# Performance work log

Hardware: AMD Instinct MI355X
Metric: run time of the kernel (lower is better)

## Reference

```python
import jax, jax.numpy as jnp
import numpy as np

NUM_HEADS = 32
NUM_KV_HEADS = 8
HEAD_DIM = 128
SCALE = 1.0 / np.sqrt(128.0)
B = 8          # num sequences
LQ = 1024 // 8 # new (query) tokens per sequence
PAGE_SIZE = 16


def setup_inputs() -> dict:
    key = jax.random.key(0)
    ks = jax.random.split(key, 5)
    q = jax.random.normal(ks[0], (B * LQ, NUM_HEADS * HEAD_DIM), dtype=jnp.float32)
    k = jax.random.normal(ks[1], (B * LQ, NUM_KV_HEADS * HEAD_DIM), dtype=jnp.float32)
    v = jax.random.normal(ks[2], (B * LQ, NUM_KV_HEADS * HEAD_DIM), dtype=jnp.float32)
    k_cache = jax.random.normal(ks[3], (1024, PAGE_SIZE, NUM_KV_HEADS, HEAD_DIM), dtype=jnp.float32)
    v_cache = jax.random.normal(ks[4], (1024, PAGE_SIZE, NUM_KV_HEADS, HEAD_DIM), dtype=jnp.float32)
    page_tables = jnp.arange(8 * 128, dtype=jnp.int64).reshape(8, 128)  # distinct pages per seq
    return {"q": q, "k": k, "v": v, "k_cache": k_cache, "v_cache": v_cache,
            "page_tables": page_tables, "ctx_len": 2048, "block_size": 32}


def reference(q, k, v, k_cache, v_cache, page_tables, ctx_len, block_size):
    nh, nkvh, hd = NUM_HEADS, NUM_KV_HEADS, HEAD_DIM
    group = nh // nkvh
    # split flat token dim into [B, Lq]
    qs = q.reshape(B, LQ, nh, hd)
    k_new = k.reshape(B, LQ, nkvh, hd)
    v_new = v.reshape(B, LQ, nkvh, hd)
    # paged gather of cached context: [B, n_pages, P, nkvh, hd] -> [B, ctx_len, nkvh, hd]
    k_ctx = k_cache[page_tables].reshape(B, ctx_len, nkvh, hd)
    v_ctx = v_cache[page_tables].reshape(B, ctx_len, nkvh, hd)
    k_full = jnp.concatenate([k_ctx, k_new], axis=1)  # [B, ctx_len+Lq, nkvh, hd]
    v_full = jnp.concatenate([v_ctx, v_new], axis=1)
    # GQA: repeat kv heads to match query heads (repeat_interleave over head dim)
    k_rep = jnp.repeat(k_full, group, axis=2)  # [B, K, nh, hd]
    v_rep = jnp.repeat(v_full, group, axis=2)
    scores = jnp.einsum('bqhd,bkhd->bhqk', qs, k_rep) * SCALE  # [B, nh, Lq, K]
    # diffusion block-causal mask over the new-token region; cache region fully visible
    qi = jnp.arange(LQ)
    abs_q = ctx_len + qi
    abs_k_new = ctx_len + jnp.arange(LQ)
    block_ends = (abs_q // block_size + 1) * block_size
    new_mask = abs_k_new[None, :] < block_ends[:, None]            # [Lq, Lq]
    cache_mask = jnp.ones((LQ, ctx_len), dtype=bool)
    mask = jnp.concatenate([cache_mask, new_mask], axis=1)         # [Lq, ctx_len+Lq]
    neg = jnp.finfo(scores.dtype).min
    scores = jnp.where(mask[None, None, :, :], scores, neg)
    probs = jax.nn.softmax(scores, axis=-1)
    out = jnp.einsum('bhqk,bkhd->bqhd', probs, v_rep)  # [B, Lq, nh, hd]
    return out.reshape(B * LQ, nh * hd).astype(q.dtype)
```

## Files before the change

### kernel.cpp

```cpp
#include <hip/hip_runtime.h>
#include <math.h>

#define NH 32
#define NKVH 8
#define GRP 4
#define HD 128
#define LQB 128
#define B_SEQ 8
#define PTSTRIDE 128
#define KVROW (NKVH * HD)
#define QK_SCALE 0.08838834764831845f
#define LOG2E 1.4426950408889634f
#define DEFER_THR 8.0f
#define NROWS (B_SEQ * LQB * NH)

typedef __attribute__((ext_vector_type(8))) __bf16 bf16x8;
typedef __attribute__((ext_vector_type(4))) __bf16 bf16x4;
typedef __attribute__((ext_vector_type(4))) float f32x4;

#define KS_BYTES 8192
#define VT_STRIDE 80
#define VT_BYTES 10240
#define KS_OFF(b) ((b) * KS_BYTES)
#define VT_OFF(b) (2 * KS_BYTES + (b) * VT_BYTES)

static __device__ __forceinline__ bf16x8 cvt8s(const float* __restrict__ p, float s) {
    const f32x4 a = *reinterpret_cast<const f32x4*>(p);
    const f32x4 b = *reinterpret_cast<const f32x4*>(p + 4);
    bf16x8 r;
    r[0] = (__bf16)(a[0] * s); r[1] = (__bf16)(a[1] * s);
    r[2] = (__bf16)(a[2] * s); r[3] = (__bf16)(a[3] * s);
    r[4] = (__bf16)(b[0] * s); r[5] = (__bf16)(b[1] * s);
    r[6] = (__bf16)(b[2] * s); r[7] = (__bf16)(b[3] * s);
    return r;
}

template<bool SPLIT>
__global__ __launch_bounds__(256, 4)
void attn_fwd(const float* __restrict__ Q,
              const float* __restrict__ Kn,
              const float* __restrict__ Vn,
              const float* __restrict__ Kc,
              const float* __restrict__ Vc,
              const int* __restrict__ PT,
              const int* __restrict__ CTX,
              float* __restrict__ O,
              float* __restrict__ WA,
              float2* __restrict__ WML)
{
    __shared__ __align__(16) unsigned char smem[2 * KS_BYTES + 2 * VT_BYTES];

    const int ctx  = CTX[0];
    const int tid  = (int)threadIdx.x;
    const int wave = tid >> 6;
    const int lane = tid & 63;
    const int low  = lane & 15;
    const int hi   = lane >> 4;

    const int bid   = (int)blockIdx.x;
    const int kvh   = bid & 7;
    const int b     = (bid >> 3) & 7;
    const int qtile = (bid >> 6) & 7;
    const int sk    = SPLIT ? (bid >> 9) : 0;
    const int head  = kvh * GRP + wave;
    const int q0    = qtile * 16;

    const int qtok = b * LQB + q0 + low;
    const float* qrow = Q + (size_t)qtok * (NH * HD) + head * HD;

    bf16x8 qf[4];
    #pragma unroll
    for (int c = 0; c < 4; ++c) qf[c] = cvt8s(qrow + 32 * c + 8 * hi, QK_SCALE * LOG2E);

    f32x4 acc[8];
    #pragma unroll
    for (int c = 0; c < 8; ++c) acc[c] = (f32x4){0.f, 0.f, 0.f, 0.f};
    float mrun = -1e30f, lrun = 0.f;

    const int vis  = ctx + (((q0 >> 5) + 1) << 5);
    const int c0   = (ctx >> 1) & ~31;
    const int kbeg = (SPLIT && sk) ? c0 : 0;
    const int kend = SPLIT ? (sk ? vis : c0) : vis;
    const int nsteps = (kend - kbeg) >> 5;

    const int skey = tid >> 3;
    const int sc8  = tid & 7;
    const int kxr  = (skey & 15) << 4;
    const int vdc  = tid >> 3;
    const int vkq  = tid & 7;

    f32x4 kr[4], vr[4];

    auto issue_loads = [&](int t0) {
        {
            const int tok = t0 + skey;
            const float* src; size_t ro;
            if (tok < ctx) {
                const int pg = PT[b * PTSTRIDE + (tok >> 4)];
                src = Kc; ro = ((size_t)pg * 16 + (tok & 15)) * KVROW + kvh * HD;
            } else {
                src = Kn; ro = (size_t)(b * LQB + tok - ctx) * KVROW + kvh * HD;
            }
            const f32x4* p = reinterpret_cast<const f32x4*>(src + ro + 16 * sc8);
            kr[0] = p[0]; kr[1] = p[1]; kr[2] = p[2]; kr[3] = p[3];
        }
        {
            const int tok0 = t0 + 4 * vkq;
            const float* src; size_t ro;
            if (tok0 < ctx) {
                const int pg = PT[b * PTSTRIDE + (tok0 >> 4)];
                src = Vc; ro = ((size_t)pg * 16 + (tok0 & 15)) * KVROW + kvh * HD;
            } else {
                src = Vn; ro = (size_t)(b * LQB + tok0 - ctx) * KVROW + kvh * HD;
            }
            const float* base = src + ro + 4 * vdc;
            vr[0] = *reinterpret_cast<const f32x4*>(base);
            vr[1] = *reinterpret_cast<const f32x4*>(base + KVROW);
            vr[2] = *reinterpret_cast<const f32x4*>(base + 2 * KVROW);
            vr[3] = *reinterpret_cast<const f32x4*>(base + 3 * KVROW);
        }
    };

    auto write_tile = [&](int buf) {
        unsigned char* ks = smem + KS_OFF(buf) + skey * 256;
        bf16x8 c0w, c1w;
        #pragma unroll
        for (int j = 0; j < 4; ++j) {
            c0w[j] = (__bf16)kr[0][j]; c0w[j + 4] = (__bf16)kr[1][j];
            c1w[j] = (__bf16)kr[2][j]; c1w[j + 4] = (__bf16)kr[3][j];
        }
        *reinterpret_cast<bf16x8*>(ks + ((32 * sc8) ^ kxr))      = c0w;
        *reinterpret_cast<bf16x8*>(ks + ((32 * sc8 + 16) ^ kxr)) = c1w;
        unsigned char* vt = smem + VT_OFF(buf) + 8 * vkq;
        #pragma unroll
        for (int di = 0; di < 4; ++di) {
            bf16x4 w;
            w[0] = (__bf16)vr[0][di]; w[1] = (__bf16)vr[1][di];
            w[2] = (__bf16)vr[2][di]; w[3] = (__bf16)vr[3][di];
            *reinterpret_cast<bf16x4*>(vt + (4 * vdc + di) * VT_STRIDE) = w;
        }
    };

    if (nsteps > 0) {
        issue_loads(kbeg);
        write_tile(0);
        __syncthreads();

        int cur = 0;
        for (int s = 0; s < nsteps; ++s) {
            if (s + 1 < nsteps) issue_loads(kbeg + ((s + 1) << 5));

            const unsigned char* ks = smem + KS_OFF(cur);
            const unsigned char* vt = smem + VT_OFF(cur);
            const int xr = low << 4;

            f32x4 s0 = (f32x4){0.f, 0.f, 0.f, 0.f};
            f32x4 s1 = (f32x4){0.f, 0.f, 0.f, 0.f};
            #pragma unroll
            for (int c = 0; c < 4; ++c) {
                bf16x8 ka = *reinterpret_cast<const bf16x8*>(ks + low * 256 + ((64 * c + 16 * hi) ^ xr));
                bf16x8 kb = *reinterpret_cast<const bf16x8*>(ks + (16 + low) * 256 + ((64 * c + 16 * hi) ^ xr));
                s0 = __builtin_amdgcn_mfma_f32_16x16x32_bf16(ka, qf[c], s0, 0, 0, 0);
                s1 = __builtin_amdgcn_mfma_f32_16x16x32_bf16(kb, qf[c], s1, 0, 0, 0);
            }

            float pmax = fmaxf(fmaxf(fmaxf(s0[0], s0[1]), fmaxf(s0[2], s0[3])),
                               fmaxf(fmaxf(s1[0], s1[1]), fmaxf(s1[2], s1[3])));

            if (!__all(pmax - mrun <= DEFER_THR)) {
                float pm = fmaxf(pmax, __shfl_xor(pmax, 16));
                pm = fmaxf(pm, __shfl_xor(pm, 32));
                const float mnew = fmaxf(mrun, pm);
                const float corr = exp2f(mrun - mnew);
                mrun = mnew;
                lrun *= corr;
                #pragma unroll
                for (int c = 0; c < 8; ++c) acc[c] *= corr;
            }

            float p[8];
            #pragma unroll
            for (int j = 0; j < 4; ++j) {
                p[j]     = exp2f(s0[j] - mrun);
                p[j + 4] = exp2f(s1[j] - mrun);
            }
            lrun += (((p[0] + p[1]) + (p[2] + p[3])) + ((p[4] + p[5]) + (p[6] + p[7])));

            bf16x8 pf;
            #pragma unroll
            for (int j = 0; j < 8; ++j) pf[j] = (__bf16)p[j];

            #pragma unroll
            for (int c = 0; c < 8; ++c) {
                const unsigned char* vrow = vt + (16 * c + low) * VT_STRIDE + 8 * hi;
                bf16x4 a0 = *reinterpret_cast<const bf16x4*>(vrow);
                bf16x4 a1 = *reinterpret_cast<const bf16x4*>(vrow + 32);
                bf16x8 vf;
                vf[0] = a0[0]; vf[1] = a0[1]; vf[2] = a0[2]; vf[3] = a0[3];
                vf[4] = a1[0]; vf[5] = a1[1]; vf[6] = a1[2]; vf[7] = a1[3];
                acc[c] = __builtin_amdgcn_mfma_f32_16x16x32_bf16(vf, pf, acc[c], 0, 0, 0);
            }

            if (s + 1 < nsteps) write_tile(cur ^ 1);
            __syncthreads();
            cur ^= 1;
        }
    }

    lrun += __shfl_xor(lrun, 16);
    lrun += __shfl_xor(lrun, 32);

    const int r = qtok * NH + head;
    if (SPLIT) {
        float* oa = WA + ((size_t)sk * NROWS + r) * HD;
        #pragma unroll
        for (int c = 0; c < 8; ++c)
            *reinterpret_cast<f32x4*>(oa + 16 * c + 4 * hi) = acc[c];
        if (hi == 0) WML[sk * NROWS + r] = make_float2(mrun, lrun);
    } else {
        const float inv = 1.0f / lrun;
        float* orow = O + (size_t)r * HD;
        #pragma unroll
        for (int c = 0; c < 8; ++c) {
            f32x4 v = acc[c] * inv;
            *reinterpret_cast<f32x4*>(orow + 16 * c + 4 * hi) = v;
        }
    }
}

__global__ __launch_bounds__(256)
void combine(const float* __restrict__ WA, const float2* __restrict__ WML,
             float* __restrict__ O)
{
    const int idx = (int)blockIdx.x * 256 + (int)threadIdx.x;
    const int r  = idx >> 5;
    const int dq = idx & 31;
    const float2 ml0 = WML[r];
    const float2 ml1 = WML[NROWS + r];
    const float M  = fmaxf(ml0.x, ml1.x);
    const float e0 = exp2f(ml0.x - M);
    const float e1 = exp2f(ml1.x - M);
    const float inv = 1.0f / (ml0.y * e0 + ml1.y * e1);
    const f32x4 a0 = *reinterpret_cast<const f32x4*>(WA + (size_t)r * HD + 4 * dq);
    const f32x4 a1 = *reinterpret_cast<const f32x4*>(WA + ((size_t)NROWS + r) * HD + 4 * dq);
    f32x4 o = (a0 * e0 + a1 * e1) * inv;
    *reinterpret_cast<f32x4*>(O + (size_t)r * HD + 4 * dq) = o;
}

extern "C" void kernel_launch(void* const* d_in, const int* in_sizes, int n_in,
                              void* d_out, int out_size, void* d_ws, size_t ws_size,
                              hipStream_t stream) {
    const float* q  = (const float*)d_in[0];
    const float* k  = (const float*)d_in[1];
    const float* v  = (const float*)d_in[2];
    const float* kc = (const float*)d_in[3];
    const float* vc = (const float*)d_in[4];
    const int*   pt = (const int*)d_in[5];
    const int*   cx = (const int*)d_in[6];
    float* out = (float*)d_out;

    const size_t wa_bytes = (size_t)2 * NROWS * HD * sizeof(float);
    const size_t needed   = wa_bytes + (size_t)2 * NROWS * sizeof(float2);

    if (ws_size >= needed) {
        float*  wa  = (float*)d_ws;
        float2* wml = (float2*)((char*)d_ws + wa_bytes);
        attn_fwd<true><<<dim3(1024), dim3(256), 0, stream>>>(q, k, v, kc, vc, pt, cx, out, wa, wml);
        combine<<<dim3(NROWS * 32 / 256), dim3(256), 0, stream>>>(wa, wml, out);
    } else {
        attn_fwd<false><<<dim3(512), dim3(256), 0, stream>>>(q, k, v, kc, vc, pt, cx, out,
                                                             nullptr, nullptr);
    }
}
```

Baseline: 271.5 us.

## Process two query tiles per wave and split KV range four ways

Each wave now handles 32 query rows (two 16-row MFMA tiles) against each shared K/V tile, halving K/V staging traffic per query. The key range is split evenly into four chunks by tile count instead of two fixed halves, keeping the grid at 1024 blocks. The K and V shared-memory writes are split so they interleave with the two MFMA phases, and setprio is raised around the matrix ops. In exchange, register pressure roughly doubles (occupancy hint drops to 3), and the combine pass must read four partial results instead of two.

After: 397.5 us. 46.4% more time.

```diff
diff --git a/kernel.cpp b/kernel.cpp
--- a/kernel.cpp
+++ b/kernel.cpp
@@ -35,8 +35,8 @@
     return r;
 }
 
-template<bool SPLIT>
-__global__ __launch_bounds__(256, 4)
+template<int NSPLIT>
+__global__ __launch_bounds__(256, 3)
 void attn_fwd(const float* __restrict__ Q,
               const float* __restrict__ Kn,
               const float* __restrict__ Vn,
@@ -60,27 +60,34 @@
     const int bid   = (int)blockIdx.x;
     const int kvh   = bid & 7;
     const int b     = (bid >> 3) & 7;
-    const int qtile = (bid >> 6) & 7;
-    const int sk    = SPLIT ? (bid >> 9) : 0;
+    const int qtile = (bid >> 6) & 3;
+    const int sk    = bid >> 8;
     const int head  = kvh * GRP + wave;
-    const int q0    = qtile * 16;
+    const int q0    = qtile * 32;
 
     const int qtok = b * LQB + q0 + low;
-    const float* qrow = Q + (size_t)qtok * (NH * HD) + head * HD;
-
-    bf16x8 qf[4];
-    #pragma unroll
-    for (int c = 0; c < 4; ++c) qf[c] = cvt8s(qrow + 32 * c + 8 * hi, QK_SCALE * LOG2E);
-
-    f32x4 acc[8];
-    #pragma unroll
-    for (int c = 0; c < 8; ++c) acc[c] = (f32x4){0.f, 0.f, 0.f, 0.f};
-    float mrun = -1e30f, lrun = 0.f;
-
-    const int vis  = ctx + (((q0 >> 5) + 1) << 5);
-    const int c0   = (ctx >> 1) & ~31;
-    const int kbeg = (SPLIT && sk) ? c0 : 0;
-    const int kend = SPLIT ? (sk ? vis : c0) : vis;
+    const float* qrow0 = Q + (size_t)qtok * (NH * HD) + head * HD;
+    const float* qrow1 = qrow0 + 16 * (NH * HD);
+
+    bf16x8 qf0[4], qf1[4];
+    #pragma unroll
+    for (int c = 0; c < 4; ++c) {
+        qf0[c] = cvt8s(qrow0 + 32 * c + 8 * hi, QK_SCALE * LOG2E);
+        qf1[c] = cvt8s(qrow1 + 32 * c + 8 * hi, QK_SCALE * LOG2E);
+    }
+
+    f32x4 acc0[8], acc1[8];
+    #pragma unroll
+    for (int c = 0; c < 8; ++c) {
+        acc0[c] = (f32x4){0.f, 0.f, 0.f, 0.f};
+        acc1[c] = (f32x4){0.f, 0.f, 0.f, 0.f};
+    }
+    float m0 = -1e30f, l0 = 0.f, m1 = -1e30f, l1 = 0.f;
+
+    const int vis  = ctx + q0 + 32;
+    const int nt   = vis >> 5;
+    const int kbeg = ((nt * sk) / NSPLIT) << 5;
+    const int kend = ((nt * (sk + 1)) / NSPLIT) << 5;
     const int nsteps = (kend - kbeg) >> 5;
 
     const int skey = tid >> 3;
@@ -121,7 +128,7 @@
         }
     };
 
-    auto write_tile = [&](int buf) {
+    auto write_k = [&](int buf) {
         unsigned char* ks = smem + KS_OFF(buf) + skey * 256;
         bf16x8 c0w, c1w;
         #pragma unroll
@@ -131,6 +138,8 @@
         }
         *reinterpret_cast<bf16x8*>(ks + ((32 * sc8) ^ kxr))      = c0w;
         *reinterpret_cast<bf16x8*>(ks + ((32 * sc8 + 16) ^ kxr)) = c1w;
+    };
+    auto write_v = [&](int buf) {
         unsigned char* vt = smem + VT_OFF(buf) + 8 * vkq;
         #pragma unroll
         for (int di = 0; di < 4; ++di) {
@@ -141,93 +150,117 @@
         }
     };
 
-    if (nsteps > 0) {
-        issue_loads(kbeg);
-        write_tile(0);
+    issue_loads(kbeg);
+    write_k(0); write_v(0);
+    __syncthreads();
+
+    int cur = 0;
+    for (int s = 0; s < nsteps; ++s) {
+        if (s + 1 < nsteps) issue_loads(kbeg + ((s + 1) << 5));
+
+        const unsigned char* ks = smem + KS_OFF(cur);
+        const unsigned char* vt = smem + VT_OFF(cur);
+        const int xr = low << 4;
+
+        f32x4 s00 = (f32x4){0.f,0.f,0.f,0.f}, s01 = (f32x4){0.f,0.f,0.f,0.f};
+        f32x4 s10 = (f32x4){0.f,0.f,0.f,0.f}, s11 = (f32x4){0.f,0.f,0.f,0.f};
+        __builtin_amdgcn_s_setprio(1);
+        #pragma unroll
+        for (int c = 0; c < 4; ++c) {
+            bf16x8 ka = *reinterpret_cast<const bf16x8*>(ks + low * 256 + ((64 * c + 16 * hi) ^ xr));
+            bf16x8 kb = *reinterpret_cast<const bf16x8*>(ks + (16 + low) * 256 + ((64 * c + 16 * hi) ^ xr));
+            s00 = __builtin_amdgcn_mfma_f32_16x16x32_bf16(ka, qf0[c], s00, 0, 0, 0);
+            s01 = __builtin_amdgcn_mfma_f32_16x16x32_bf16(kb, qf0[c], s01, 0, 0, 0);
+            s10 = __builtin_amdgcn_mfma_f32_16x16x32_bf16(ka, qf1[c], s10, 0, 0, 0);
+            s11 = __builtin_amdgcn_mfma_f32_16x16x32_bf16(kb, qf1[c], s11, 0, 0, 0);
+        }
+        __builtin_amdgcn_s_setprio(0);
+
+        if (s + 1 < nsteps) write_k(cur ^ 1);
+
+        float pm0 = fmaxf(fmaxf(fmaxf(s00[0], s00[1]), fmaxf(s00[2], s00[3])),
+                          fmaxf(fmaxf(s01[0], s01[1]), fmaxf(s01[2], s01[3])));
+        float pm1 = fmaxf(fmaxf(fmaxf(s10[0], s10[1]), fmaxf(s10[2], s10[3])),
+                          fmaxf(fmaxf(s11[0], s11[1]), fmaxf(s11[2], s11[3])));
+
+        if (!__all((pm0 - m0 <= DEFER_THR) && (pm1 - m1 <= DEFER_THR))) {
+            float r0 = fmaxf(pm0, __shfl_xor(pm0, 16));
+            r0 = fmaxf(r0, __shfl_xor(r0, 32));
+            float r1 = fmaxf(pm1, __shfl_xor(pm1, 16));
+            r1 = fmaxf(r1, __shfl_xor(r1, 32));
+            const float n0 = fmaxf(m0, r0), n1 = fmaxf(m1, r1);
+            const float c0f = exp2f(m0 - n0), c1f = exp2f(m1 - n1);
+            m0 = n0; m1 = n1;
+            l0 *= c0f; l1 *= c1f;
+            #pragma unroll
+            for (int c = 0; c < 8; ++c) { acc0[c] *= c0f; acc1[c] *= c1f; }
+        }
+
+        float p0[8], p1[8];
+        #pragma unroll
+        for (int j = 0; j < 4; ++j) {
+            p0[j]     = exp2f(s00[j] - m0);
+            p0[j + 4] = exp2f(s01[j] - m0);
+            p1[j]     = exp2f(s10[j] - m1);
+            p1[j + 4] = exp2f(s11[j] - m1);
+        }
+        l0 += ((p0[0] + p0[1]) + (p0[2] + p0[3])) + ((p0[4] + p0[5]) + (p0[6] + p0[7]));
+        l1 += ((p1[0] + p1[1]) + (p1[2] + p1[3])) + ((p1[4] + p1[5]) + (p1[6] + p1[7]));
+
+        bf16x8 pf0, pf1;
+        #pragma unroll
+        for (int j = 0; j < 8; ++j) { pf0[j] = (__bf16)p0[j]; pf1[j] = (__bf16)p1[j]; }
+
+        __builtin_amdgcn_s_setprio(1);
+        #pragma unroll
+        for (int c = 0; c < 8; ++c) {
+            const unsigned char* vrow = vt + (16 * c + low) * VT_STRIDE + 8 * hi;
+            bf16x4 a0 = *reinterpret_cast<const bf16x4*>(vrow);
+            bf16x4 a1 = *reinterpret_cast<const bf16x4*>(vrow + 32);
+            bf16x8 vf;
+            vf[0] = a0[0]; vf[1] = a0[1]; vf[2] = a0[2]; vf[3] = a0[3];
+            vf[4] = a1[0]; vf[5] = a1[1]; vf[6] = a1[2]; vf[7] = a1[3];
+            acc0[c] = __builtin_amdgcn_mfma_f32_16x16x32_bf16(vf, pf0, acc0[c], 0, 0, 0);
+            acc1[c] = __builtin_amdgcn_mfma_f32_16x16x32_bf16(vf, pf1, acc1[c], 0, 0, 0);
+        }
+        __builtin_amdgcn_s_setprio(0);
+
+        if (s + 1 < nsteps) write_v(cur ^ 1);
         __syncthreads();
-
-        int cur = 0;
-        for (int s = 0; s < nsteps; ++s) {
-            if (s + 1 < nsteps) issue_loads(kbeg + ((s + 1) << 5));
-
-            const unsigned char* ks = smem + KS_OFF(cur);
-            const unsigned char* vt = smem + VT_OFF(cur);
-            const int xr = low << 4;
-
-            f32x4 s0 = (f32x4){0.f, 0.f, 0.f, 0.f};
-            f32x4 s1 = (f32x4){0.f, 0.f, 0.f, 0.f};
-            #pragma unroll
-            for (int c = 0; c < 4; ++c) {
-                bf16x8 ka = *reinterpret_cast<const bf16x8*>(ks + low * 256 + ((64 * c + 16 * hi) ^ xr));
-                bf16x8 kb = *reinterpret_cast<const bf16x8*>(ks + (16 + low) * 256 + ((64 * c + 16 * hi) ^ xr));
-                s0 = __builtin_amdgcn_mfma_f32_16x16x32_bf16(ka, qf[c], s0, 0, 0, 0);
-                s1 = __builtin_amdgcn_mfma_f32_16x16x32_bf16(kb, qf[c], s1, 0, 0, 0);
-            }
-
-            float pmax = fmaxf(fmaxf(fmaxf(s0[0], s0[1]), fmaxf(s0[2], s0[3])),
-                               fmaxf(fmaxf(s1[0], s1[1]), fmaxf(s1[2], s1[3])));
-
-            if (!__all(pmax - mrun <= DEFER_THR)) {
-                float pm = fmaxf(pmax, __shfl_xor(pmax, 16));
-                pm = fmaxf(pm, __shfl_xor(pm, 32));
-                const float mnew = fmaxf(mrun, pm);
-                const float corr = exp2f(mrun - mnew);
-                mrun = mnew;
-                lrun *= corr;
-                #pragma unroll
-                for (int c = 0; c < 8; ++c) acc[c] *= corr;
-            }
-
-            float p[8];
-            #pragma unroll
-            for (int j = 0; j < 4; ++j) {
-                p[j]     = exp2f(s0[j] - mrun);
-                p[j + 4] = exp2f(s1[j] - mrun);
-            }
-            lrun += (((p[0] + p[1]) + (p[2] + p[3])) + ((p[4] + p[5]) + (p[6] + p[7])));
-
-            bf16x8 pf;
-            #pragma unroll
-            for (int j = 0; j < 8; ++j) pf[j] = (__bf16)p[j];
-
-            #pragma unroll
-            for (int c = 0; c < 8; ++c) {
-                const unsigned char* vrow = vt + (16 * c + low) * VT_STRIDE + 8 * hi;
-                bf16x4 a0 = *reinterpret_cast<const bf16x4*>(vrow);
-                bf16x4 a1 = *reinterpret_cast<const bf16x4*>(vrow + 32);
-                bf16x8 vf;
-                vf[0] = a0[0]; vf[1] = a0[1]; vf[2] = a0[2]; vf[3] = a0[3];
-                vf[4] = a1[0]; vf[5] = a1[1]; vf[6] = a1[2]; vf[7] = a1[3];
-                acc[c] = __builtin_amdgcn_mfma_f32_16x16x32_bf16(vf, pf, acc[c], 0, 0, 0);
-            }
-
-            if (s + 1 < nsteps) write_tile(cur ^ 1);
-            __syncthreads();
-            cur ^= 1;
-        }
-    }
-
-    lrun += __shfl_xor(lrun, 16);
-    lrun += __shfl_xor(lrun, 32);
-
-    const int r = qtok * NH + head;
-    if (SPLIT) {
-        float* oa = WA + ((size_t)sk * NROWS + r) * HD;
-        #pragma unroll
-        for (int c = 0; c < 8; ++c)
-            *reinterpret_cast<f32x4*>(oa + 16 * c + 4 * hi) = acc[c];
-        if (hi == 0) WML[sk * NROWS + r] = make_float2(mrun, lrun);
+        cur ^= 1;
+    }
+
+    l0 += __shfl_xor(l0, 16); l0 += __shfl_xor(l0, 32);
+    l1 += __shfl_xor(l1, 16); l1 += __shfl_xor(l1, 32);
+
+    const int r0 = qtok * NH + head;
+    const int r1 = r0 + 16 * NH;
+    if (NSPLIT > 1) {
+        float* oa0 = WA + ((size_t)sk * NROWS + r0) * HD;
+        float* oa1 = WA + ((size_t)sk * NROWS + r1) * HD;
+        #pragma unroll
+        for (int c = 0; c < 8; ++c) {
+            *reinterpret_cast<f32x4*>(oa0 + 16 * c + 4 * hi) = acc0[c];
+            *reinterpret_cast<f32x4*>(oa1 + 16 * c + 4 * hi) = acc1[c];
+        }
+        if (hi == 0) {
+            WML[sk * NROWS + r0] = make_float2(m0, l0);
+            WML[sk * NROWS + r1] = make_float2(m1, l1);
+        }
     } else {
-        const float inv = 1.0f / lrun;
-        float* orow = O + (size_t)r * HD;
+        const float i0 = 1.0f / l0, i1 = 1.0f / l1;
+        float* o0 = O + (size_t)r0 * HD;
+        float* o1 = O + (size_t)r1 * HD;
         #pragma unroll
         for (int c = 0; c < 8; ++c) {
-            f32x4 v = acc[c] * inv;
-            *reinterpret_cast<f32x4*>(orow + 16 * c + 4 * hi) = v;
+            f32x4 v0 = acc0[c] * i0, v1 = acc1[c] * i1;
+            *reinterpret_cast<f32x4*>(o0 + 16 * c + 4 * hi) = v0;
+            *reinterpret_cast<f32x4*>(o1 + 16 * c + 4 * hi) = v1;
         }
     }
 }
 
+template<int NSPLIT>
 __global__ __launch_bounds__(256)
 void combine(const float* __restrict__ WA, const float2* __restrict__ WML,
              float* __restrict__ O)
@@ -235,15 +268,22 @@
     const int idx = (int)blockIdx.x * 256 + (int)threadIdx.x;
     const int r  = idx >> 5;
     const int dq = idx & 31;
-    const float2 ml0 = WML[r];
-    const float2 ml1 = WML[NROWS + r];
-    const float M  = fmaxf(ml0.x, ml1.x);
-    const float e0 = exp2f(ml0.x - M);
-    const float e1 = exp2f(ml1.x - M);
-    const float inv = 1.0f / (ml0.y * e0 + ml1.y * e1);
-    const f32x4 a0 = *reinterpret_cast<const f32x4*>(WA + (size_t)r * HD + 4 * dq);
-    const f32x4 a1 = *reinterpret_cast<const f32x4*>(WA + ((size_t)NROWS + r) * HD + 4 * dq);
-    f32x4 o = (a0 * e0 + a1 * e1) * inv;
+    float2 ml[NSPLIT];
+    float M = -1e30f;
+    #pragma unroll
+    for (int s = 0; s < NSPLIT; ++s) { ml[s] = WML[s * NROWS + r]; M = fmaxf(M, ml[s].x); }
+    float e[NSPLIT];
+    float den = 0.f;
+    #pragma unroll
+    for (int s = 0; s < NSPLIT; ++s) { e[s] = exp2f(ml[s].x - M); den += ml[s].y * e[s]; }
+    const float inv = 1.0f / den;
+    f32x4 o = (f32x4){0.f, 0.f, 0.f, 0.f};
+    #pragma unroll
+    for (int s = 0; s < NSPLIT; ++s) {
+        const f32x4 a = *reinterpret_cast<const f32x4*>(WA + ((size_t)s * NROWS + r) * HD + 4 * dq);
+        o += a * e[s];
+    }
+    o *= inv;
     *reinterpret_cast<f32x4*>(O + (size_t)r * HD + 4 * dq) = o;
 }
 
@@ -259,16 +299,23 @@
     const int*   cx = (const int*)d_in[6];
     float* out = (float*)d_out;
 
-    const size_t wa_bytes = (size_t)2 * NROWS * HD * sizeof(float);
-    const size_t needed   = wa_bytes + (size_t)2 * NROWS * sizeof(float2);
-
-    if (ws_size >= needed) {
+    const size_t wa4 = (size_t)4 * NROWS * HD * sizeof(float);
+    const size_t need4 = wa4 + (size_t)4 * NROWS * sizeof(float2);
+    const size_t wa2 = (size_t)2 * NROWS * HD * sizeof(float);
+    const size_t need2 = wa2 + (size_t)2 * NROWS * sizeof(float2);
+
+    if (ws_size >= need4) {
         float*  wa  = (float*)d_ws;
-        float2* wml = (float2*)((char*)d_ws + wa_bytes);
-        attn_fwd<true><<<dim3(1024), dim3(256), 0, stream>>>(q, k, v, kc, vc, pt, cx, out, wa, wml);
-        combine<<<dim3(NROWS * 32 / 256), dim3(256), 0, stream>>>(wa, wml, out);
+        float2* wml = (float2*)((char*)d_ws + wa4);
+        attn_fwd<4><<<dim3(1024), dim3(256), 0, stream>>>(q, k, v, kc, vc, pt, cx, out, wa, wml);
+        combine<4><<<dim3(NROWS * 32 / 256), dim3(256), 0, stream>>>(wa, wml, out);
+    } else if (ws_size >= need2) {
+        float*  wa  = (float*)d_ws;
+        float2* wml = (float2*)((char*)d_ws + wa2);
+        attn_fwd<2><<<dim3(512), dim3(256), 0, stream>>>(q, k, v, kc, vc, pt, cx, out, wa, wml);
+        combine<2><<<dim3(NROWS * 32 / 256), dim3(256), 0, stream>>>(wa, wml, out);
     } else {
-        attn_fwd<false><<<dim3(512), dim3(256), 0, stream>>>(q, k, v, kc, vc, pt, cx, out,
-                                                             nullptr, nullptr);
+        attn_fwd<1><<<dim3(256), dim3(256), 0, stream>>>(q, k, v, kc, vc, pt, cx, out,
+                                                         nullptr, nullptr);
     }
 }
```

## Deepen K/V prefetch pipeline to two tiles and balance split-KV ranges

Applied to the files above, without the earlier changes.

The main loop now keeps two global-load stages in flight: the next tile is written to shared memory at the start of each step and loads for the tile after that are issued immediately. The __syncthreads is replaced by an lgkmcnt wait plus a raw s_barrier, and the final barrier is skipped. Split boundaries are now computed by dividing the visible tile count evenly rather than halving the context, which balances work between the two splits, and the split count is templated. This hides more global-load latency behind compute at the cost of more live registers for the in-flight loads.

Measured after the change: 270.7 us. About the same (-0.3%).

```diff
diff --git a/kernel.cpp b/kernel.cpp
--- a/kernel.cpp
+++ b/kernel.cpp
@@ -35,7 +35,7 @@
     return r;
 }
 
-template<bool SPLIT>
+template<int NSPLIT>
 __global__ __launch_bounds__(256, 4)
 void attn_fwd(const float* __restrict__ Q,
               const float* __restrict__ Kn,
@@ -61,7 +61,7 @@
     const int kvh   = bid & 7;
     const int b     = (bid >> 3) & 7;
     const int qtile = (bid >> 6) & 7;
-    const int sk    = SPLIT ? (bid >> 9) : 0;
+    const int sk    = (NSPLIT > 1) ? (bid >> 9) : 0;
     const int head  = kvh * GRP + wave;
     const int q0    = qtile * 16;
 
@@ -78,9 +78,9 @@
     float mrun = -1e30f, lrun = 0.f;
 
     const int vis  = ctx + (((q0 >> 5) + 1) << 5);
-    const int c0   = (ctx >> 1) & ~31;
-    const int kbeg = (SPLIT && sk) ? c0 : 0;
-    const int kend = SPLIT ? (sk ? vis : c0) : vis;
+    const int nt   = vis >> 5;
+    const int kbeg = ((nt * sk) / NSPLIT) << 5;
+    const int kend = ((nt * (sk + 1)) / NSPLIT) << 5;
     const int nsteps = (kend - kbeg) >> 5;
 
     const int skey = tid >> 3;
@@ -141,77 +141,81 @@
         }
     };
 
-    if (nsteps > 0) {
-        issue_loads(kbeg);
-        write_tile(0);
-        __syncthreads();
-
-        int cur = 0;
-        for (int s = 0; s < nsteps; ++s) {
-            if (s + 1 < nsteps) issue_loads(kbeg + ((s + 1) << 5));
-
-            const unsigned char* ks = smem + KS_OFF(cur);
-            const unsigned char* vt = smem + VT_OFF(cur);
-            const int xr = low << 4;
-
-            f32x4 s0 = (f32x4){0.f, 0.f, 0.f, 0.f};
-            f32x4 s1 = (f32x4){0.f, 0.f, 0.f, 0.f};
+    auto tile_barrier = [&]() {
+        asm volatile("s_waitcnt lgkmcnt(0)" ::: "memory");
+        __builtin_amdgcn_s_barrier();
+    };
+
+    issue_loads(kbeg);
+    write_tile(0);
+    if (nsteps > 1) issue_loads(kbeg + 32);
+    tile_barrier();
+
+    int cur = 0;
+    for (int s = 0; s < nsteps; ++s) {
+        if (s + 1 < nsteps) write_tile(cur ^ 1);
+        if (s + 2 < nsteps) issue_loads(kbeg + ((s + 2) << 5));
+
+        const unsigned char* ks = smem + KS_OFF(cur);
+        const unsigned char* vt = smem + VT_OFF(cur);
+        const int xr = low << 4;
+
+        f32x4 s0 = (f32x4){0.f, 0.f, 0.f, 0.f};
+        f32x4 s1 = (f32x4){0.f, 0.f, 0.f, 0.f};
+        #pragma unroll
+        for (int c = 0; c < 4; ++c) {
+            bf16x8 ka = *reinterpret_cast<const bf16x8*>(ks + low * 256 + ((64 * c + 16 * hi) ^ xr));
+            bf16x8 kb = *reinterpret_cast<const bf16x8*>(ks + (16 + low) * 256 + ((64 * c + 16 * hi) ^ xr));
+            s0 = __builtin_amdgcn_mfma_f32_16x16x32_bf16(ka, qf[c], s0, 0, 0, 0);
+            s1 = __builtin_amdgcn_mfma_f32_16x16x32_bf16(kb, qf[c], s1, 0, 0, 0);
+        }
+
+        float pmax = fmaxf(fmaxf(fmaxf(s0[0], s0[1]), fmaxf(s0[2], s0[3])),
+                           fmaxf(fmaxf(s1[0], s1[1]), fmaxf(s1[2], s1[3])));
+
+        if (!__all(pmax - mrun <= DEFER_THR)) {
+            float pm = fmaxf(pmax, __shfl_xor(pmax, 16));
+            pm = fmaxf(pm, __shfl_xor(pm, 32));
+            const float mnew = fmaxf(mrun, pm);
+            const float corr = exp2f(mrun - mnew);
+            mrun = mnew;
+            lrun *= corr;
             #pragma unroll
-            for (int c = 0; c < 4; ++c) {
-                bf16x8 ka = *reinterpret_cast<const bf16x8*>(ks + low * 256 + ((64 * c + 16 * hi) ^ xr));
-                bf16x8 kb = *reinterpret_cast<const bf16x8*>(ks + (16 + low) * 256 + ((64 * c + 16 * hi) ^ xr));
-                s0 = __builtin_amdgcn_mfma_f32_16x16x32_bf16(ka, qf[c], s0, 0, 0, 0);
-                s1 = __builtin_amdgcn_mfma_f32_16x16x32_bf16(kb, qf[c], s1, 0, 0, 0);
-            }
-
-            float pmax = fmaxf(fmaxf(fmaxf(s0[0], s0[1]), fmaxf(s0[2], s0[3])),
-                               fmaxf(fmaxf(s1[0], s1[1]), fmaxf(s1[2], s1[3])));
-
-            if (!__all(pmax - mrun <= DEFER_THR)) {
-                float pm = fmaxf(pmax, __shfl_xor(pmax, 16));
-                pm = fmaxf(pm, __shfl_xor(pm, 32));
-                const float mnew = fmaxf(mrun, pm);
-                const float corr = exp2f(mrun - mnew);
-                mrun = mnew;
-                lrun *= corr;
-                #pragma unroll
-                for (int c = 0; c < 8; ++c) acc[c] *= corr;
-            }
-
-            float p[8];
-            #pragma unroll
-            for (int j = 0; j < 4; ++j) {
-                p[j]     = exp2f(s0[j] - mrun);
-                p[j + 4] = exp2f(s1[j] - mrun);
-            }
-            lrun += (((p[0] + p[1]) + (p[2] + p[3])) + ((p[4] + p[5]) + (p[6] + p[7])));
-
-            bf16x8 pf;
-            #pragma unroll
-            for (int j = 0; j < 8; ++j) pf[j] = (__bf16)p[j];
-
-            #pragma unroll
-            for (int c = 0; c < 8; ++c) {
-                const unsigned char* vrow = vt + (16 * c + low) * VT_STRIDE + 8 * hi;
-                bf16x4 a0 = *reinterpret_cast<const bf16x4*>(vrow);
-                bf16x4 a1 = *reinterpret_cast<const bf16x4*>(vrow + 32);
-                bf16x8 vf;
-                vf[0] = a0[0]; vf[1] = a0[1]; vf[2] = a0[2]; vf[3] = a0[3];
-                vf[4] = a1[0]; vf[5] = a1[1]; vf[6] = a1[2]; vf[7] = a1[3];
-                acc[c] = __builtin_amdgcn_mfma_f32_16x16x32_bf16(vf, pf, acc[c], 0, 0, 0);
-            }
-
-            if (s + 1 < nsteps) write_tile(cur ^ 1);
-            __syncthreads();
-            cur ^= 1;
-        }
+            for (int c = 0; c < 8; ++c) acc[c] *= corr;
+        }
+
+        float p[8];
+        #pragma unroll
+        for (int j = 0; j < 4; ++j) {
+            p[j]     = exp2f(s0[j] - mrun);
+            p[j + 4] = exp2f(s1[j] - mrun);
+        }
+        lrun += (((p[0] + p[1]) + (p[2] + p[3])) + ((p[4] + p[5]) + (p[6] + p[7])));
+
+        bf16x8 pf;
+        #pragma unroll
+        for (int j = 0; j < 8; ++j) pf[j] = (__bf16)p[j];
+
+        #pragma unroll
+        for (int c = 0; c < 8; ++c) {
+            const unsigned char* vrow = vt + (16 * c + low) * VT_STRIDE + 8 * hi;
+            bf16x4 a0 = *reinterpret_cast<const bf16x4*>(vrow);
+            bf16x4 a1 = *reinterpret_cast<const bf16x4*>(vrow + 32);
+            bf16x8 vf;
+            vf[0] = a0[0]; vf[1] = a0[1]; vf[2] = a0[2]; vf[3] = a0[3];
+            vf[4] = a1[0]; vf[5] = a1[1]; vf[6] = a1[2]; vf[7] = a1[3];
+            acc[c] = __builtin_amdgcn_mfma_f32_16x16x32_bf16(vf, pf, acc[c], 0, 0, 0);
+        }
+
+        if (s + 1 < nsteps) tile_barrier();
+        cur ^= 1;
     }
 
     lrun += __shfl_xor(lrun, 16);
     lrun += __shfl_xor(lrun, 32);
 
     const int r = qtok * NH + head;
-    if (SPLIT) {
+    if (NSPLIT > 1) {
         float* oa = WA + ((size_t)sk * NROWS + r) * HD;
         #pragma unroll
         for (int c = 0; c < 8; ++c)
@@ -228,6 +232,7 @@
     }
 }
 
+template<int NSPLIT>
 __global__ __launch_bounds__(256)
 void combine(const float* __restrict__ WA, const float2* __restrict__ WML,
              float* __restrict__ O)
@@ -235,15 +240,22 @@
     const int idx = (int)blockIdx.x * 256 + (int)threadIdx.x;
     const int r  = idx >> 5;
     const int dq = idx & 31;
-    const float2 ml0 = WML[r];
-    const float2 ml1 = WML[NROWS + r];
-    const float M  = fmaxf(ml0.x, ml1.x);
-    const float e0 = exp2f(ml0.x - M);
-    const float e1 = exp2f(ml1.x - M);
-    const float inv = 1.0f / (ml0.y * e0 + ml1.y * e1);
-    const f32x4 a0 = *reinterpret_cast<const f32x4*>(WA + (size_t)r * HD + 4 * dq);
-    const f32x4 a1 = *reinterpret_cast<const f32x4*>(WA + ((size_t)NROWS + r) * HD + 4 * dq);
-    f32x4 o = (a0 * e0 + a1 * e1) * inv;
+    float2 ml[NSPLIT];
+    float M = -1e30f;
+    #pragma unroll
+    for (int s = 0; s < NSPLIT; ++s) { ml[s] = WML[s * NROWS + r]; M = fmaxf(M, ml[s].x); }
+    float e[NSPLIT];
+    float den = 0.f;
+    #pragma unroll
+    for (int s = 0; s < NSPLIT; ++s) { e[s] = exp2f(ml[s].x - M); den += ml[s].y * e[s]; }
+    const float inv = 1.0f / den;
+    f32x4 o = (f32x4){0.f, 0.f, 0.f, 0.f};
+    #pragma unroll
+    for (int s = 0; s < NSPLIT; ++s) {
+        const f32x4 a = *reinterpret_cast<const f32x4*>(WA + ((size_t)s * NROWS + r) * HD + 4 * dq);
+        o += a * e[s];
+    }
+    o *= inv;
     *reinterpret_cast<f32x4*>(O + (size_t)r * HD + 4 * dq) = o;
 }
 
@@ -259,16 +271,16 @@
     const int*   cx = (const int*)d_in[6];
     float* out = (float*)d_out;
 
-    const size_t wa_bytes = (size_t)2 * NROWS * HD * sizeof(float);
-    const size_t needed   = wa_bytes + (size_t)2 * NROWS * sizeof(float2);
-
-    if (ws_size >= needed) {
+    const size_t wa2   = (size_t)2 * NROWS * HD * sizeof(float);
+    const size_t need2 = wa2 + (size_t)2 * NROWS * sizeof(float2);
+
+    if (ws_size >= need2) {
         float*  wa  = (float*)d_ws;
-        float2* wml = (float2*)((char*)d_ws + wa_bytes);
-        attn_fwd<true><<<dim3(1024), dim3(256), 0, stream>>>(q, k, v, kc, vc, pt, cx, out, wa, wml);
-        combine<<<dim3(NROWS * 32 / 256), dim3(256), 0, stream>>>(wa, wml, out);
+        float2* wml = (float2*)((char*)d_ws + wa2);
+        attn_fwd<2><<<dim3(1024), dim3(256), 0, stream>>>(q, k, v, kc, vc, pt, cx, out, wa, wml);
+        combine<2><<<dim3(NROWS * 32 / 256), dim3(256), 0, stream>>>(wa, wml, out);
     } else {
-        attn_fwd<false><<<dim3(512), dim3(256), 0, stream>>>(q, k, v, kc, vc, pt, cx, out,
-                                                             nullptr, nullptr);
-    }
-}
+        attn_fwd<1><<<dim3(512), dim3(256), 0, stream>>>(q, k, v, kc, vc, pt, cx, out,
+                                                         nullptr, nullptr);
+    }
+}
```
